# Performance work log

Measured on AMD Instinct MI355X. Metric: run time of the kernel, lower is better.

## Reference

```python
import jax, jax.numpy as jnp
import numpy as np

N_NODES = 1_000_000
N_EDGES = 4_000_000  # knn_k = 4
N_GRAPHS = 1024
HIDDEN = 64
N_FEAT = 4


def setup_inputs() -> dict:
    key = jax.random.key(0)
    k0, k1, k2, k3, k4 = jax.random.split(key, 5)
    x = jax.random.normal(k0, (N_NODES, N_FEAT), dtype=jnp.float32)
    edge_index = jax.random.randint(k1, (2, N_EDGES), 0, N_NODES, dtype=jnp.int64)
    batch = jnp.sort(jax.random.randint(k2, (N_NODES,), 0, N_GRAPHS, dtype=jnp.int64))
    W1 = jax.random.normal(k3, (N_FEAT, HIDDEN), dtype=jnp.float32) * 0.5
    b1 = jnp.zeros((HIDDEN,), dtype=jnp.float32)
    W2 = jax.random.normal(k4, (HIDDEN, 1), dtype=jnp.float32) * 0.1
    b2 = jnp.zeros((1,), dtype=jnp.float32)
    return {"x": x, "W1": W1, "b1": b1, "W2": W2, "b2": b2,
            "edge_index": edge_index, "batch": batch}


def gcn_conv(x, edge_index, W, b):
    # PyG GCNConv: linear transform, add self-loops, sym-normalize, scatter-add.
    n = x.shape[0]
    h = x @ W  # [N, 64]
    loop = jnp.arange(n, dtype=edge_index.dtype)
    row = jnp.concatenate([edge_index[0], loop])  # source j
    col = jnp.concatenate([edge_index[1], loop])  # target i
    deg = jax.ops.segment_sum(jnp.ones_like(col, dtype=h.dtype), col, num_segments=n)
    dis = jnp.where(deg > 0, jax.lax.rsqrt(jnp.maximum(deg, 1.0)), 0.0)
    norm = dis[row] * dis[col]  # [E+N]
    out = jax.ops.segment_sum(h[row] * norm[:, None], col, num_segments=n)
    return out + b


def reference(x, W1, b1, W2, b2, edge_index, batch):
    h = gcn_conv(x, edge_index, W1, b1)          # [N, 64]
    h = jax.nn.elu(h)                            # ELU activation
    pooled = jax.ops.segment_sum(h, batch, num_segments=N_GRAPHS)  # global_add_pool
    return pooled @ W2 + b2                      # [G, 1]
```

## Files before the change

### kernel.cpp

```cpp
#include <hip/hip_runtime.h>
#include <hip/hip_fp16.h>

#define N_NODES 1000000
#define N_EDGES 4000000
#define N_GRAPHS 1024
#define HIDDEN 64

#define G1 250
#define T1 512
#define EPB (N_EDGES / G1)
#define EPB4 (EPB / 4)
#define BSHIFT 11
#define BSIZE 2048
#define NBK 512
#define NBUCK ((N_NODES + BSIZE - 1) / BSIZE)

typedef int      vi4 __attribute__((ext_vector_type(4)));
typedef unsigned vu4 __attribute__((ext_vector_type(4)));

__device__ __forceinline__ int4 nt_int4(const int4* p) {
    vi4 v = __builtin_nontemporal_load((const vi4*)p);
    return make_int4(v.x, v.y, v.z, v.w);
}
__device__ __forceinline__ uint4 nt_uint4(const uint4* p) {
    vu4 v = __builtin_nontemporal_load((const vu4*)p);
    return make_uint4(v.x, v.y, v.z, v.w);
}

__global__ __launch_bounds__(T1) void k_hist(const int4* __restrict__ col4,
                                             int* __restrict__ part,
                                             float* __restrict__ out,
                                             const float* __restrict__ b2) {
    __shared__ int h[NBK];
    int t = threadIdx.x, blk = blockIdx.x;
    for (int i = t; i < NBK; i += T1) h[i] = 0;
    int gid = blk * T1 + t;
    if (gid < N_GRAPHS) out[gid] = b2[0];
    __syncthreads();
    int b0 = blk * EPB4;
    for (int i = t; i < EPB4; i += T1) {
        int4 c = nt_int4(col4 + b0 + i);
        atomicAdd(&h[((unsigned)c.x) >> BSHIFT], 1);
        atomicAdd(&h[((unsigned)c.y) >> BSHIFT], 1);
        atomicAdd(&h[((unsigned)c.z) >> BSHIFT], 1);
        atomicAdd(&h[((unsigned)c.w) >> BSHIFT], 1);
    }
    __syncthreads();
    for (int i = t; i < NBK; i += T1) part[blk * NBK + i] = h[i];
}

__global__ __launch_bounds__(256) void k_colscan(int* __restrict__ part,
                                                 int* __restrict__ ecnt) {
    int b = blockIdx.x;
    int t = threadIdx.x;
    __shared__ int a[256];
    int v = (t < G1) ? part[t * NBK + b] : 0;
    a[t] = v;
    __syncthreads();
    for (int o = 1; o < 256; o <<= 1) {
        int u = (t >= o) ? a[t - o] : 0;
        __syncthreads();
        a[t] += u;
        __syncthreads();
    }
    if (t < G1) part[t * NBK + b] = a[t] - v;
    if (t == 255) ecnt[b] = a[255];
}

__global__ __launch_bounds__(NBK) void k_bscan(const int* __restrict__ ecnt,
                                               int* __restrict__ ebase) {
    __shared__ int sc[NBK];
    int b = threadIdx.x;
    int run4 = (ecnt[b] + 3) & ~3;
    sc[b] = run4;
    __syncthreads();
    for (int o = 1; o < NBK; o <<= 1) {
        int v = (b >= o) ? sc[b - o] : 0;
        __syncthreads();
        sc[b] += v;
        __syncthreads();
    }
    ebase[b] = sc[b] - run4;
}

__global__ __launch_bounds__(T1) void k_part(const int4* __restrict__ row4,
                                             const int4* __restrict__ col4,
                                             const int* __restrict__ part,
                                             const int* __restrict__ ebase,
                                             unsigned* __restrict__ epair) {
    __shared__ int cur[NBK];
    int t = threadIdx.x, blk = blockIdx.x;
    for (int i = t; i < NBK; i += T1) cur[i] = part[blk * NBK + i] + ebase[i];
    __syncthreads();
    int b0 = blk * EPB4;
    for (int i = t; i < EPB4; i += T1) {
        int4 c = nt_int4(col4 + b0 + i);
        int4 r = nt_int4(row4 + b0 + i);
        int cc[4] = {c.x, c.y, c.z, c.w};
        int rr[4] = {r.x, r.y, r.z, r.w};
        #pragma unroll
        for (int k = 0; k < 4; ++k) {
            int b = ((unsigned)cc[k]) >> BSHIFT;
            int pos = atomicAdd(&cur[b], 1);
            epair[pos] = ((unsigned)(cc[k] & (BSIZE - 1)) << 20) | (unsigned)rr[k];
        }
    }
}

__global__ __launch_bounds__(1024) void k_deg2(const unsigned* __restrict__ epair,
                                               const int* __restrict__ ebase,
                                               const int* __restrict__ ecnt,
                                               const float4* __restrict__ x,
                                               float* __restrict__ dis,
                                               uint2* __restrict__ xdh) {
    __shared__ int deg[BSIZE];
    int t = threadIdx.x, b = blockIdx.x;
    for (int i = t; i < BSIZE; i += 1024) deg[i] = 1;
    __syncthreads();
    int ne = ecnt[b];
    const unsigned* ep = epair + ebase[b];
    int ne4 = ne & ~3;
    for (int i = 4 * t; i < ne4; i += 4096) {
        uint4 u = nt_uint4((const uint4*)(ep + i));
        atomicAdd(&deg[u.x >> 20], 1);
        atomicAdd(&deg[u.y >> 20], 1);
        atomicAdd(&deg[u.z >> 20], 1);
        atomicAdd(&deg[u.w >> 20], 1);
    }
    for (int i = ne4 + t; i < ne; i += 1024) atomicAdd(&deg[ep[i] >> 20], 1);
    __syncthreads();
    int n0 = b << BSHIFT;
    for (int i = t; i < BSIZE; i += 1024) {
        int node = n0 + i;
        if (node < N_NODES) {
            float d = rsqrtf((float)deg[i]);
            dis[node] = d;
            float4 xv = x[node];
            __half2 h01 = __floats2half2_rn(xv.x * d, xv.y * d);
            __half2 h23 = __floats2half2_rn(xv.z * d, xv.w * d);
            uint2 pk;
            pk.x = *(unsigned*)&h01;
            pk.y = *(unsigned*)&h23;
            xdh[node] = pk;
        }
    }
}

__device__ __forceinline__ void acc_edge(unsigned u, uint2 p, float* sf) {
    int loc = u >> 20;
    __half2 h01 = *(__half2*)&p.x;
    __half2 h23 = *(__half2*)&p.y;
    float2 f01 = __half22float2(h01);
    float2 f23 = __half22float2(h23);
    float* sp = sf + loc * 5;
    atomicAdd(sp + 0, f01.x);
    atomicAdd(sp + 1, f01.y);
    atomicAdd(sp + 2, f23.x);
    atomicAdd(sp + 3, f23.y);
}

__global__ __launch_bounds__(1024) void k_accF(const unsigned* __restrict__ epair,
                                               const int* __restrict__ ebase,
                                               const int* __restrict__ ecnt,
                                               const uint2* __restrict__ xdh,
                                               const float* __restrict__ dis,
                                               const int* __restrict__ batch,
                                               const float* __restrict__ W1,
                                               const float* __restrict__ b1,
                                               const float* __restrict__ W2,
                                               float* __restrict__ out) {
    __shared__ float sf[BSIZE * 5];
    int t = threadIdx.x, b = blockIdx.x;
    for (int i = t; i < BSIZE * 5; i += 1024) sf[i] = 0.f;
    __syncthreads();
    int ne = ecnt[b];
    const unsigned* ep = epair + ebase[b];
    int ne4 = ne & ~3;
    for (int i = 4 * t; i < ne4; i += 4096) {
        unsigned u0 = ep[i], u1 = ep[i + 1], u2 = ep[i + 2], u3 = ep[i + 3];
        uint2 p0 = xdh[u0 & 0xFFFFFu];
        uint2 p1 = xdh[u1 & 0xFFFFFu];
        uint2 p2 = xdh[u2 & 0xFFFFFu];
        uint2 p3 = xdh[u3 & 0xFFFFFu];
        acc_edge(u0, p0, sf);
        acc_edge(u1, p1, sf);
        acc_edge(u2, p2, sf);
        acc_edge(u3, p3, sf);
    }
    for (int i = ne4 + t; i < ne; i += 1024) {
        unsigned u = ep[i];
        acc_edge(u, xdh[u & 0xFFFFFu], sf);
    }
    __syncthreads();
    int n0 = b << BSHIFT;
    #pragma unroll
    for (int k = 0; k < BSIZE / 1024; ++k) {
        int ln = t + k * 1024;
        int node = n0 + ln;
        bool valid = node < N_NODES;
        float acc = 0.f;
        int g = -1;
        if (valid) {
            const float* sp = sf + ln * 5;
            uint2 p = xdh[node];
            __half2 h01 = *(__half2*)&p.x;
            __half2 h23 = *(__half2*)&p.y;
            float2 f01 = __half22float2(h01);
            float2 f23 = __half22float2(h23);
            float d = dis[node];
            float u0 = d * (sp[0] + f01.x);
            float u1 = d * (sp[1] + f01.y);
            float u2 = d * (sp[2] + f23.x);
            float u3 = d * (sp[3] + f23.y);
            g = batch[node];
            #pragma unroll
            for (int kk = 0; kk < HIDDEN; ++kk) {
                float tt = fmaf(u0, W1[kk],
                           fmaf(u1, W1[HIDDEN + kk],
                           fmaf(u2, W1[2 * HIDDEN + kk],
                           fmaf(u3, W1[3 * HIDDEN + kk], b1[kk]))));
                float h = tt > 0.f ? tt : (__expf(tt) - 1.f);
                acc = fmaf(h, W2[kk], acc);
            }
        }
        unsigned long long rem = __ballot(valid);
        while (rem) {
            int leader = __ffsll(rem) - 1;
            int gl = __shfl(g, leader);
            bool mine = valid && (g == gl);
            unsigned long long mask = __ballot(mine);
            float v = mine ? acc : 0.f;
            #pragma unroll
            for (int o = 32; o; o >>= 1) v += __shfl_xor(v, o);
            if ((int)(t & 63) == leader) unsafeAtomicAdd(&out[gl], v);
            rem &= ~mask;
        }
    }
}

__global__ __launch_bounds__(256) void k_init(int* __restrict__ deg, float4* __restrict__ s,
                                              float* __restrict__ out, const float* __restrict__ b2) {
    int i = blockIdx.x * blockDim.x + threadIdx.x;
    if (i < N_NODES) { deg[i] = 1; s[i] = make_float4(0.f, 0.f, 0.f, 0.f); }
    if (i < N_GRAPHS) out[i] = b2[0];
}
__global__ __launch_bounds__(256) void k_deg(const int* __restrict__ col, int* __restrict__ deg) {
    int e = blockIdx.x * blockDim.x + threadIdx.x;
    if (e < N_EDGES) atomicAdd(&deg[col[e]], 1);
}
__global__ __launch_bounds__(256) void k_dis(const int* __restrict__ deg, float* __restrict__ dis) {
    int i = blockIdx.x * blockDim.x + threadIdx.x;
    if (i < N_NODES) dis[i] = rsqrtf((float)deg[i]);
}
__global__ __launch_bounds__(256) void k_scatter(const int* __restrict__ row, const int* __restrict__ col,
                                                 const float4* __restrict__ x, const float* __restrict__ dis,
                                                 float* __restrict__ s) {
    int e = blockIdx.x * blockDim.x + threadIdx.x;
    if (e >= N_EDGES) return;
    int j = row[e], i = col[e];
    float dj = dis[j];
    float4 xj = x[j];
    float* sp = s + 4ll * (long long)i;
    unsafeAtomicAdd(sp + 0, xj.x * dj);
    unsafeAtomicAdd(sp + 1, xj.y * dj);
    unsafeAtomicAdd(sp + 2, xj.z * dj);
    unsafeAtomicAdd(sp + 3, xj.w * dj);
}
__global__ __launch_bounds__(256) void k_node(const float4* __restrict__ x, const float4* __restrict__ s,
                                              const float* __restrict__ dis, const int* __restrict__ batch,
                                              const float* __restrict__ W1, const float* __restrict__ b1,
                                              const float* __restrict__ W2, float* __restrict__ out) {
    int n = blockIdx.x * blockDim.x + threadIdx.x;
    bool valid = n < N_NODES;
    float acc = 0.f; int g = -1;
    if (valid) {
        float4 xn = x[n], sn = s[n];
        float di = dis[n], inv = di * di;
        float u0 = di * sn.x + inv * xn.x, u1 = di * sn.y + inv * xn.y;
        float u2 = di * sn.z + inv * xn.z, u3 = di * sn.w + inv * xn.w;
        g = batch[n];
        #pragma unroll
        for (int k = 0; k < HIDDEN; ++k) {
            float t = fmaf(u0, W1[k], fmaf(u1, W1[HIDDEN + k],
                      fmaf(u2, W1[2 * HIDDEN + k], fmaf(u3, W1[3 * HIDDEN + k], b1[k]))));
            float h = t > 0.f ? t : expm1f(t);
            acc = fmaf(h, W2[k], acc);
        }
    }
    unsigned long long rem = __ballot(valid);
    while (rem) {
        int leader = __ffsll(rem) - 1;
        int gl = __shfl(g, leader);
        bool mine = valid && (g == gl);
        unsigned long long mask = __ballot(mine);
        float v = mine ? acc : 0.f;
        #pragma unroll
        for (int o = 32; o; o >>= 1) v += __shfl_xor(v, o);
        if ((int)(threadIdx.x & 63) == leader) unsafeAtomicAdd(&out[gl], v);
        rem &= ~mask;
    }
}

extern "C" void kernel_launch(void* const* d_in, const int* in_sizes, int n_in,
                              void* d_out, int out_size, void* d_ws, size_t ws_size,
                              hipStream_t stream) {
    const float* x   = (const float*)d_in[0];
    const float* W1  = (const float*)d_in[1];
    const float* b1  = (const float*)d_in[2];
    const float* W2  = (const float*)d_in[3];
    const float* b2  = (const float*)d_in[4];
    const int*   ei  = (const int*)d_in[5];
    const int*   bat = (const int*)d_in[6];
    float* out = (float*)d_out;

    const int* row = ei;
    const int* col = ei + N_EDGES;
    char* ws = (char*)d_ws;

    size_t o_ep   = 0;
    size_t o_xdh  = o_ep + (size_t)(N_EDGES + 4 * NBK) * 4;
    size_t o_dis  = o_xdh + (size_t)N_NODES * 8;
    size_t o_part = o_dis + (size_t)N_NODES * 4;
    size_t o_eb   = o_part + (size_t)G1 * NBK * 4;
    size_t o_ec   = o_eb + NBK * 4;
    size_t need   = o_ec + NBK * 4;

    if (ws_size >= need) {
        unsigned* epair = (unsigned*)(ws + o_ep);
        uint2*    xdh   = (uint2*)(ws + o_xdh);
        float*    dis   = (float*)(ws + o_dis);
        int*      part  = (int*)(ws + o_part);
        int*      ebase = (int*)(ws + o_eb);
        int*      ecnt  = (int*)(ws + o_ec);

        k_hist<<<G1, T1, 0, stream>>>((const int4*)col, part, out, b2);
        k_colscan<<<NBK, 256, 0, stream>>>(part, ecnt);
        k_bscan<<<1, NBK, 0, stream>>>(ecnt, ebase);
        k_part<<<G1, T1, 0, stream>>>((const int4*)row, (const int4*)col, part, ebase, epair);
        k_deg2<<<NBUCK, 1024, 0, stream>>>(epair, ebase, ecnt, (const float4*)x, dis, xdh);
        k_accF<<<NBUCK, 1024, 0, stream>>>(epair, ebase, ecnt, xdh, dis, bat, W1, b1, W2, out);
    } else {
        int nb_n = (N_NODES + 255) / 256;
        int nb_e = (N_EDGES + 255) / 256;
        int*    deg = (int*)(ws);
        float*  dis = (float*)(ws + (size_t)N_NODES * 4);
        float*  s   = (float*)(ws + (size_t)N_NODES * 8);
        float4* s4  = (float4*)s;
        k_init<<<nb_n, 256, 0, stream>>>(deg, s4, out, b2);
        k_deg<<<nb_e, 256, 0, stream>>>(col, deg);
        k_dis<<<nb_n, 256, 0, stream>>>(deg, dis);
        k_scatter<<<nb_e, 256, 0, stream>>>(row, col, (const float4*)x, dis, s);
        k_node<<<nb_n, 256, 0, stream>>>((const float4*)x, s4, dis, bat, W1, b1, W2, out);
    }
}
```

Baseline: 176.5 us.

## Split fused accumulate+MLP kernel and raise histogram grid to 1000 blocks

Splits the per-bucket edge accumulation kernel from the per-node MLP/ELU/pool epilogue. Accumulated sums now go through a global float4 buffer and are consumed by a separate 256-thread kernel spread over many more blocks. This is meant to stop the 489 large shared-memory-bound blocks from serializing the heavy 64-wide MLP. It also increases the histogram/partition grid from 250 to 1000 blocks and widens the column scan to 1024 threads to get more parallelism in the bucketing phase. The cost is an extra 16 MB write and read of the intermediate buffer, one more launch, and a larger partition table.

```diff
diff --git a/kernel.cpp b/kernel.cpp
--- a/kernel.cpp
+++ b/kernel.cpp
@@ -6,7 +6,7 @@
 #define N_GRAPHS 1024
 #define HIDDEN 64
 
-#define G1 250
+#define G1 1000
 #define T1 512
 #define EPB (N_EDGES / G1)
 #define EPB4 (EPB / 4)
@@ -49,22 +49,22 @@
     for (int i = t; i < NBK; i += T1) part[blk * NBK + i] = h[i];
 }
 
-__global__ __launch_bounds__(256) void k_colscan(int* __restrict__ part,
-                                                 int* __restrict__ ecnt) {
+__global__ __launch_bounds__(1024) void k_colscan(int* __restrict__ part,
+                                                  int* __restrict__ ecnt) {
     int b = blockIdx.x;
     int t = threadIdx.x;
-    __shared__ int a[256];
+    __shared__ int a[1024];
     int v = (t < G1) ? part[t * NBK + b] : 0;
     a[t] = v;
     __syncthreads();
-    for (int o = 1; o < 256; o <<= 1) {
+    for (int o = 1; o < 1024; o <<= 1) {
         int u = (t >= o) ? a[t - o] : 0;
         __syncthreads();
         a[t] += u;
         __syncthreads();
     }
     if (t < G1) part[t * NBK + b] = a[t] - v;
-    if (t == 255) ecnt[b] = a[255];
+    if (t == 1023) ecnt[b] = a[1023];
 }
 
 __global__ __launch_bounds__(NBK) void k_bscan(const int* __restrict__ ecnt,
@@ -159,16 +159,11 @@
     atomicAdd(sp + 3, f23.y);
 }
 
-__global__ __launch_bounds__(1024) void k_accF(const unsigned* __restrict__ epair,
-                                               const int* __restrict__ ebase,
-                                               const int* __restrict__ ecnt,
-                                               const uint2* __restrict__ xdh,
-                                               const float* __restrict__ dis,
-                                               const int* __restrict__ batch,
-                                               const float* __restrict__ W1,
-                                               const float* __restrict__ b1,
-                                               const float* __restrict__ W2,
-                                               float* __restrict__ out) {
+__global__ __launch_bounds__(1024) void k_acc(const unsigned* __restrict__ epair,
+                                              const int* __restrict__ ebase,
+                                              const int* __restrict__ ecnt,
+                                              const uint2* __restrict__ xdh,
+                                              float4* __restrict__ sbuf) {
     __shared__ float sf[BSIZE * 5];
     int t = threadIdx.x, b = blockIdx.x;
     for (int i = t; i < BSIZE * 5; i += 1024) sf[i] = 0.f;
@@ -193,48 +188,61 @@
     }
     __syncthreads();
     int n0 = b << BSHIFT;
-    #pragma unroll
-    for (int k = 0; k < BSIZE / 1024; ++k) {
-        int ln = t + k * 1024;
-        int node = n0 + ln;
-        bool valid = node < N_NODES;
-        float acc = 0.f;
-        int g = -1;
-        if (valid) {
-            const float* sp = sf + ln * 5;
-            uint2 p = xdh[node];
-            __half2 h01 = *(__half2*)&p.x;
-            __half2 h23 = *(__half2*)&p.y;
-            float2 f01 = __half22float2(h01);
-            float2 f23 = __half22float2(h23);
-            float d = dis[node];
-            float u0 = d * (sp[0] + f01.x);
-            float u1 = d * (sp[1] + f01.y);
-            float u2 = d * (sp[2] + f23.x);
-            float u3 = d * (sp[3] + f23.y);
-            g = batch[node];
-            #pragma unroll
-            for (int kk = 0; kk < HIDDEN; ++kk) {
-                float tt = fmaf(u0, W1[kk],
-                           fmaf(u1, W1[HIDDEN + kk],
-                           fmaf(u2, W1[2 * HIDDEN + kk],
-                           fmaf(u3, W1[3 * HIDDEN + kk], b1[kk]))));
-                float h = tt > 0.f ? tt : (__expf(tt) - 1.f);
-                acc = fmaf(h, W2[kk], acc);
-            }
-        }
-        unsigned long long rem = __ballot(valid);
-        while (rem) {
-            int leader = __ffsll(rem) - 1;
-            int gl = __shfl(g, leader);
-            bool mine = valid && (g == gl);
-            unsigned long long mask = __ballot(mine);
-            float v = mine ? acc : 0.f;
-            #pragma unroll
-            for (int o = 32; o; o >>= 1) v += __shfl_xor(v, o);
-            if ((int)(t & 63) == leader) unsafeAtomicAdd(&out[gl], v);
-            rem &= ~mask;
-        }
+    for (int i = t; i < BSIZE; i += 1024) {
+        int node = n0 + i;
+        if (node < N_NODES) {
+            const float* q = sf + i * 5;
+            sbuf[node] = make_float4(q[0], q[1], q[2], q[3]);
+        }
+    }
+}
+
+__global__ __launch_bounds__(256) void k_mlp(const float4* __restrict__ sbuf,
+                                             const uint2* __restrict__ xdh,
+                                             const float* __restrict__ dis,
+                                             const int* __restrict__ batch,
+                                             const float* __restrict__ W1,
+                                             const float* __restrict__ b1,
+                                             const float* __restrict__ W2,
+                                             float* __restrict__ out) {
+    int n = blockIdx.x * blockDim.x + threadIdx.x;
+    bool valid = n < N_NODES;
+    float acc = 0.f;
+    int g = -1;
+    if (valid) {
+        float4 sv = sbuf[n];
+        uint2 p = xdh[n];
+        __half2 h01 = *(__half2*)&p.x;
+        __half2 h23 = *(__half2*)&p.y;
+        float2 f01 = __half22float2(h01);
+        float2 f23 = __half22float2(h23);
+        float d = dis[n];
+        float u0 = d * (sv.x + f01.x);
+        float u1 = d * (sv.y + f01.y);
+        float u2 = d * (sv.z + f23.x);
+        float u3 = d * (sv.w + f23.y);
+        g = batch[n];
+        #pragma unroll
+        for (int k = 0; k < HIDDEN; ++k) {
+            float t = fmaf(u0, W1[k],
+                      fmaf(u1, W1[HIDDEN + k],
+                      fmaf(u2, W1[2 * HIDDEN + k],
+                      fmaf(u3, W1[3 * HIDDEN + k], b1[k]))));
+            float h = t > 0.f ? t : (__expf(t) - 1.f);
+            acc = fmaf(h, W2[k], acc);
+        }
+    }
+    unsigned long long rem = __ballot(valid);
+    while (rem) {
+        int leader = __ffsll(rem) - 1;
+        int gl = __shfl(g, leader);
+        bool mine = valid && (g == gl);
+        unsigned long long mask = __ballot(mine);
+        float v = mine ? acc : 0.f;
+        #pragma unroll
+        for (int o = 32; o; o >>= 1) v += __shfl_xor(v, o);
+        if ((int)(threadIdx.x & 63) == leader) unsafeAtomicAdd(&out[gl], v);
+        rem &= ~mask;
     }
 }
 
@@ -318,7 +326,8 @@
     char* ws = (char*)d_ws;
 
     size_t o_ep   = 0;
-    size_t o_xdh  = o_ep + (size_t)(N_EDGES + 4 * NBK) * 4;
+    size_t o_sb   = o_ep + (size_t)(N_EDGES + 4 * NBK) * 4;
+    size_t o_xdh  = o_sb + (size_t)N_NODES * 16;
     size_t o_dis  = o_xdh + (size_t)N_NODES * 8;
     size_t o_part = o_dis + (size_t)N_NODES * 4;
     size_t o_eb   = o_part + (size_t)G1 * NBK * 4;
@@ -327,6 +336,7 @@
 
     if (ws_size >= need) {
         unsigned* epair = (unsigned*)(ws + o_ep);
+        float4*   sbuf  = (float4*)(ws + o_sb);
         uint2*    xdh   = (uint2*)(ws + o_xdh);
         float*    dis   = (float*)(ws + o_dis);
         int*      part  = (int*)(ws + o_part);
@@ -334,11 +344,12 @@
         int*      ecnt  = (int*)(ws + o_ec);
 
         k_hist<<<G1, T1, 0, stream>>>((const int4*)col, part, out, b2);
-        k_colscan<<<NBK, 256, 0, stream>>>(part, ecnt);
+        k_colscan<<<NBK, 1024, 0, stream>>>(part, ecnt);
         k_bscan<<<1, NBK, 0, stream>>>(ecnt, ebase);
         k_part<<<G1, T1, 0, stream>>>((const int4*)row, (const int4*)col, part, ebase, epair);
         k_deg2<<<NBUCK, 1024, 0, stream>>>(epair, ebase, ecnt, (const float4*)x, dis, xdh);
-        k_accF<<<NBUCK, 1024, 0, stream>>>(epair, ebase, ecnt, xdh, dis, bat, W1, b1, W2, out);
+        k_acc<<<NBUCK, 1024, 0, stream>>>(epair, ebase, ecnt, xdh, sbuf);
+        k_mlp<<<(N_NODES + 255) / 256, 256, 0, stream>>>(sbuf, xdh, dis, bat, W1, b1, W2, out);
     } else {
         int nb_n = (N_NODES + 255) / 256;
         int nb_e = (N_EDGES + 255) / 256;
```

Result: slower. 193.5 us (+9.7%).
